# Kernel tuning notes

Measured on AMD Instinct MI355X. Metric: run time of the kernel, lower is better.

Reference implementation:

```python
import jax, jax.numpy as jnp
import numpy as np

PATCH = 16


def setup_inputs() -> dict:
    key = jax.random.key(0)
    x = jax.random.normal(key, (256, 3, 224, 224), dtype=jnp.float32)
    return {"x": x}


def reference(x):
    P = PATCH
    B, C, Hi, Wi = x.shape
    h, w = Hi // P, Wi // P  # grid rows (h) and cols (w)
    # 'b c (h p1) (w p2) -> b w h p1 p2 c'
    patches = x.reshape(B, C, h, P, w, P).transpose(0, 4, 2, 3, 5, 1)  # (B, w, h, p1, p2, C)
    # center_rotate: transpose p1<->p2 for patches with grid col j in [w/3, 2w/3]
    # and grid row k in [h/3, 2h/3] (original skips j < W/3 or j > 2W/3, same for k)
    jw = jnp.arange(w)
    kh = jnp.arange(h)
    mw = (jw >= w / 3) & (jw <= 2 * w / 3)
    mh = (kh >= h / 3) & (kh <= 2 * h / 3)
    mask = (mw[:, None] & mh[None, :])[None, :, :, None, None, None]  # (1, w, h, 1, 1, 1)
    rot = jnp.where(mask, jnp.swapaxes(patches, 3, 4), patches)  # (B, w, h, a3, a4, C)
    # 'b w h p2 p1 c -> b c (h p2) (w p1)': axis3 is read as p2 (inner height),
    # axis4 as p1 (inner width) -- i.e. every patch gets transposed on reassembly,
    # so center patches (transposed twice) come back in original orientation.
    out = rot.transpose(0, 5, 2, 3, 1, 4).reshape(B, C, h * P, w * P)
    return out
```

## Files before the change

kernel.cpp:

```cpp
#include <hip/hip_runtime.h>


#define HH 224
#define WW 224
#define W4 56

__global__ __launch_bounds__(256) void patch_rotate_kernel(
    const float* __restrict__ x, float* __restrict__ out, int n4) {
  int idx = blockIdx.x * blockDim.x + threadIdx.x;
  if (idx >= n4) return;

  int bc   = idx / (HH * W4);
  int rem  = idx % (HH * W4);
  int row  = rem / W4;
  int col4 = rem % W4;

  int k = row >> 4;
  int j = col4 >> 2;

  bool center = (j >= 5) & (j <= 9) & (k >= 5) & (k <= 9);

  float4 v;
  if (!center) {
    v = ((const float4*)x)[idx];
  } else {
    int a3  = row & 15;
    int a4b = (col4 & 3) << 2;
    int base = (bc * HH + (k << 4)) * WW + (j << 4) + a3;
    v.x = x[base + (a4b + 0) * WW];
    v.y = x[base + (a4b + 1) * WW];
    v.z = x[base + (a4b + 2) * WW];
    v.w = x[base + (a4b + 3) * WW];
  }
  ((float4*)out)[idx] = v;
}

extern "C" void kernel_launch(void* const* d_in, const int* in_sizes, int n_in,
                              void* d_out, int out_size, void* d_ws, size_t ws_size,
                              hipStream_t stream) {
  const float* x = (const float*)d_in[0];
  float* out = (float*)d_out;
  int n4 = out_size / 4;
  int threads = 256;
  int blocks = (n4 + threads - 1) / threads;
  patch_rotate_kernel<<<blocks, threads, 0, stream>>>(x, out, n4);
}
```

Baseline: 252.9 us.

## Map one wavefront per patch and transpose center patches through LDS

The kernel changes from a flat per-float4 mapping to one 64-lane wavefront per 16x16 patch. Every lane issues a float4 load, and center patches are transposed through a padded shared-memory tile rather than gathered with strided scalar global loads. This targets the uncoalesced scalar reads in the center region. In exchange, each wave's global accesses become 64-byte row segments instead of fully contiguous spans, and every block now pays a __syncthreads even when none of its patches need transposing.

```diff
diff --git a/kernel.cpp b/kernel.cpp
--- a/kernel.cpp
+++ b/kernel.cpp
@@ -1,38 +1,39 @@
 #include <hip/hip_runtime.h>
 
 
-#define HH 224
-#define WW 224
-#define W4 56
+__global__ __launch_bounds__(256) void patch_rotate_kernel(
+    const float* __restrict__ x, float* __restrict__ out) {
+  __shared__ float lds[4 * 16 * 20];
 
-__global__ __launch_bounds__(256) void patch_rotate_kernel(
-    const float* __restrict__ x, float* __restrict__ out, int n4) {
-  int idx = blockIdx.x * blockDim.x + threadIdx.x;
-  if (idx >= n4) return;
+  int tid    = threadIdx.x;
+  int lane   = tid & 63;
+  int wavein = tid >> 6;
+  int w  = blockIdx.x * 4 + wavein;
+  int bc = w / 196;
+  int t  = w - bc * 196;
+  int k  = t / 14;
+  int j  = t - k * 14;
+  int r  = lane >> 2;
+  int c4 = lane & 3;
 
-  int bc   = idx / (HH * W4);
-  int rem  = idx % (HH * W4);
-  int row  = rem / W4;
-  int col4 = rem % W4;
-
-  int k = row >> 4;
-  int j = col4 >> 2;
+  int off = bc * 50176 + (k * 16 + r) * 224 + j * 16 + c4 * 4;
+  float4 v = *(const float4*)(x + off);
 
   bool center = (j >= 5) & (j <= 9) & (k >= 5) & (k <= 9);
+  float* my = lds + wavein * 320;
 
-  float4 v;
-  if (!center) {
-    v = ((const float4*)x)[idx];
-  } else {
-    int a3  = row & 15;
-    int a4b = (col4 & 3) << 2;
-    int base = (bc * HH + (k << 4)) * WW + (j << 4) + a3;
-    v.x = x[base + (a4b + 0) * WW];
-    v.y = x[base + (a4b + 1) * WW];
-    v.z = x[base + (a4b + 2) * WW];
-    v.w = x[base + (a4b + 3) * WW];
+  if (center) {
+    *(float4*)(my + r * 20 + c4 * 4) = v;
   }
-  ((float4*)out)[idx] = v;
+  __syncthreads();
+  if (center) {
+    int c0 = c4 * 4;
+    v.x = my[(c0 + 0) * 20 + r];
+    v.y = my[(c0 + 1) * 20 + r];
+    v.z = my[(c0 + 2) * 20 + r];
+    v.w = my[(c0 + 3) * 20 + r];
+  }
+  *(float4*)(out + off) = v;
 }
 
 extern "C" void kernel_launch(void* const* d_in, const int* in_sizes, int n_in,
@@ -40,8 +41,6 @@
                               hipStream_t stream) {
   const float* x = (const float*)d_in[0];
   float* out = (float*)d_out;
-  int n4 = out_size / 4;
-  int threads = 256;
-  int blocks = (n4 + threads - 1) / threads;
-  patch_rotate_kernel<<<blocks, threads, 0, stream>>>(x, out, n4);
+  int blocks = 150528 / 4;
+  patch_rotate_kernel<<<blocks, 256, 0, stream>>>(x, out);
 }
```

Result: slower. 259.2 us (+2.5%).
